# Performance work log

Hardware: AMD Instinct MI355X
Metric: run time of the kernel (lower is better)

Reference implementation:

```python
import jax, jax.numpy as jnp
import numpy as np

B, T, D, NH = 2, 2048, 512, 8
DK = D // NH
P = 2 * T - 1  # relative position length
INIT_SCALE = 0.02


def rel_shift(x):
    # x: [B, H, T, P] -> Transformer-XL pad/reshape shift
    b, h, t, p = x.shape
    x = jnp.pad(x, ((0, 0), (0, 0), (0, 0), (1, 0)))
    x = x.reshape(b, h, p + 1, t)[:, :, 1:]
    return x.reshape(b, h, t, p)


def setup_inputs() -> dict:
    key = jax.random.key(0)
    ks = jax.random.split(key, 7)
    return {
        "x": jax.random.normal(ks[0], (B, T, D), jnp.float32),
        "pos_emb": jax.random.normal(ks[1], (1, P, D), jnp.float32),
        "attn_mask": jnp.zeros((B, T, T), dtype=bool),
        "W_qkv": jax.random.normal(ks[2], (3 * D, D), jnp.float32) * INIT_SCALE,
        "W_pos": jax.random.normal(ks[3], (D, D), jnp.float32) * INIT_SCALE,
        "W_out": jax.random.normal(ks[4], (D, D), jnp.float32) * INIT_SCALE,
        "pos_bias_u": jax.random.normal(ks[5], (NH, DK), jnp.float32) * INIT_SCALE,
        "pos_bias_v": jax.random.normal(ks[6], (NH, DK), jnp.float32) * INIT_SCALE,
    }


def reference(x, pos_emb, attn_mask, W_qkv, W_pos, W_out, pos_bias_u, pos_bias_v):
    b, t, d = x.shape
    nh, dk = pos_bias_u.shape
    scale = 1.0 / np.sqrt(dk).astype(np.float32)
    mask = attn_mask[:, None]  # [B,1,T,T], True = masked

    qkv = x @ W_qkv.T  # [B,T,3D]
    q, k, v = jnp.split(qkv, 3, axis=-1)
    q = q.reshape(b, t, nh, dk)                       # [B,T,H,dk]
    k = k.reshape(b, t, nh, dk).transpose(0, 2, 1, 3)  # [B,H,T,dk]
    v = v.reshape(b, t, nh, dk).transpose(0, 2, 1, 3)  # [B,H,T,dk]

    # pos_emb batch dim is 1 -> squeeze
    pos = (pos_emb @ W_pos.T).reshape(-1, nh, dk).transpose(1, 0, 2)  # [H,P,dk]

    q_u = (q + pos_bias_u).transpose(0, 2, 1, 3)  # [B,H,T,dk]
    q_v = (q + pos_bias_v).transpose(0, 2, 1, 3)  # [B,H,T,dk]

    # relative-position bias: [B,H,T,P] -> shift -> slice to key length
    bd = jnp.einsum("bhtd,hpd->bhtp", q_v, pos)
    bd = rel_shift(bd)[..., :t] * scale
    bd = jnp.where(mask, jnp.float32(-100000.0), bd)

    # SDPA with additive bias (scale = 1/sqrt(dk), matching torch default)
    scores = jnp.einsum("bhtd,bhsd->bhts", q_u, k) * scale + bd
    attn = jax.nn.softmax(scores, axis=-1)
    out = jnp.einsum("bhts,bhsd->bhtd", attn, v)
    out = out.transpose(0, 2, 1, 3)  # [B,T,H,dk]

    # zero fully-masked query rows
    fully_masked = jnp.all(mask, axis=-1)[:, 0]  # [B,T]
    out = jnp.where(fully_masked[:, :, None, None], 0.0, out)

    out = out.reshape(b, t, nh * dk)
    return out @ W_out.T
```

## Files before the change

### kernel.cpp

```cpp
#include <hip/hip_runtime.h>
#include <hip/hip_bf16.h>


typedef __attribute__((ext_vector_type(8))) short short8;
typedef __attribute__((ext_vector_type(16))) float f32x16;
typedef __attribute__((ext_vector_type(4))) float f32x4;
typedef __attribute__((ext_vector_type(2))) unsigned int uint2v;

#define C2F 0.18033688011112043f
#define MOFF 144269.504088896f

static __device__ __forceinline__ unsigned short f2bf(float x) {
    unsigned int u = __builtin_bit_cast(unsigned int, x);
    u += 0x7FFFu + ((u >> 16) & 1u);
    return (unsigned short)(u >> 16);
}
static __device__ __forceinline__ unsigned int cvt2bf(float lo, float hi) {
    __hip_bfloat162 h = __float22bfloat162_rn(make_float2(lo, hi));
    unsigned int r;
    __builtin_memcpy(&r, &h, 4);
    return r;
}
static __device__ __forceinline__ float exp2v(float x) {
    return __builtin_amdgcn_exp2f(x);
}
static __device__ __forceinline__ float bf2f(unsigned short u) {
    return __builtin_bit_cast(float, (unsigned int)u << 16);
}
static __device__ __forceinline__ f32x16 zero16() {
    f32x16 v;
#pragma unroll
    for (int i = 0; i < 16; ++i) v[i] = 0.0f;
    return v;
}
static __device__ __forceinline__ f32x16 mfma_bf(short8 a, short8 b, f32x16 c) {
    return __builtin_amdgcn_mfma_f32_32x32x16_bf16(a, b, c, 0, 0, 0);
}
static __device__ __forceinline__ short8 load8f(const float* base, size_t eoff) {
    const float4* p = (const float4*)(base + eoff);
    float4 a = p[0], b = p[1];
    union { unsigned int u[4]; short8 s; } r;
    r.u[0] = cvt2bf(a.x, a.y);
    r.u[1] = cvt2bf(a.z, a.w);
    r.u[2] = cvt2bf(b.x, b.y);
    r.u[3] = cvt2bf(b.z, b.w);
    return r.s;
}

__global__ __launch_bounds__(256) void front_kernel(
    const float* __restrict__ x, const float* __restrict__ wqkv,
    const float* __restrict__ pe, const float* __restrict__ wpos,
    unsigned short* __restrict__ qu, unsigned short* __restrict__ qv,
    unsigned short* __restrict__ kb, unsigned short* __restrict__ vt,
    unsigned short* __restrict__ posb,
    const float* __restrict__ bu, const float* __restrict__ bv,
    const unsigned char* __restrict__ mk, unsigned long long* __restrict__ mwout)
{
    const int tid = threadIdx.x;
    const int bid = blockIdx.x;

    if (bid >= 512) {
        int base = (bid - 512) * 256 + tid;
#pragma unroll 1
        for (int idx = base; idx < 131072; idx += 32768) {
            const unsigned long long* row =
                (const unsigned long long*)(mk + (size_t)(idx >> 5) * 2048) +
                (size_t)(idx & 31) * 8;
            unsigned long long w = 0;
#pragma unroll
            for (int k = 0; k < 8; ++k) {
                unsigned long long v = row[k];
                v |= v >> 4; v |= v >> 2; v |= v >> 1;
                v &= 0x0101010101010101ull;
                w |= ((v * 0x0102040810204080ull) >> 56) << (k * 8);
            }
            mwout[idx] = w;
        }
        return;
    }

    const int role = bid >= 384 ? 1 : 0;
    const int lb = role ? bid - 384 : bid;
    const int bx = role ? (lb & 3) : (lb % 12);
    const int by = role ? (lb >> 2) : (lb / 12);
    const float* A  = role ? pe : x;
    const float* Bw = role ? wpos : wqkv;
    const int M = role ? 4095 : 4096;

    __shared__ __align__(16) unsigned short As[128 * 32];
    __shared__ __align__(16) unsigned short Bs[128 * 32];

    const int lane = tid & 63;
    const int l31 = lane & 31;
    const int h = (lane >> 5) & 1;
    const int wid = tid >> 6;
    const int wm = wid >> 1, wn = wid & 1;
    const int m0 = by * 128, n0 = bx * 128;

    f32x16 acc[2][2];
#pragma unroll
    for (int mt = 0; mt < 2; ++mt)
#pragma unroll
        for (int nt = 0; nt < 2; ++nt) acc[mt][nt] = zero16();

    const int row_s = tid >> 2;
    const int q_s = tid & 3;

#pragma unroll 1
    for (int k0 = 0; k0 < 512; k0 += 32) {
        __syncthreads();
#pragma unroll
        for (int rep = 0; rep < 2; ++rep) {
            int row = row_s + rep * 64;
            int ar = m0 + row; if (ar > M - 1) ar = M - 1;
            short8 av = load8f(A, (size_t)ar * 512 + k0 + q_s * 8);
            *(short8*)((char*)As + ((row * 64 + q_s * 16) ^ ((row & 3) << 4))) = av;
            int br = n0 + row;
            short8 bv8 = load8f(Bw, (size_t)br * 512 + k0 + q_s * 8);
            *(short8*)((char*)Bs + ((row * 64 + q_s * 16) ^ ((row & 3) << 4))) = bv8;
        }
        __syncthreads();

        short8 af[2][2], bf[2][2];
#pragma unroll
        for (int mt = 0; mt < 2; ++mt)
#pragma unroll
            for (int ks = 0; ks < 2; ++ks) {
                int row = wm * 64 + mt * 32 + l31;
                af[mt][ks] = *(const short8*)((char*)As +
                    ((row * 64 + ks * 32 + h * 16) ^ ((row & 3) << 4)));
            }
#pragma unroll
        for (int nt = 0; nt < 2; ++nt)
#pragma unroll
            for (int ks = 0; ks < 2; ++ks) {
                int row = wn * 64 + nt * 32 + l31;
                bf[nt][ks] = *(const short8*)((char*)Bs +
                    ((row * 64 + ks * 32 + h * 16) ^ ((row & 3) << 4)));
            }
#pragma unroll
        for (int mt = 0; mt < 2; ++mt)
#pragma unroll
            for (int nt = 0; nt < 2; ++nt)
#pragma unroll
                for (int ks = 0; ks < 2; ++ks)
                    acc[mt][nt] = mfma_bf(af[mt][ks], bf[nt][ks], acc[mt][nt]);
    }

#pragma unroll
    for (int mt = 0; mt < 2; ++mt)
#pragma unroll
        for (int nt = 0; nt < 2; ++nt) {
            int Ncol = n0 + wn * 64 + nt * 32 + l31;
#pragma unroll
            for (int r = 0; r < 16; ++r) {
                int Mrow = m0 + wm * 64 + mt * 32 + (r & 3) + ((r >> 2) << 3) + h * 4;
                float v = acc[mt][nt][r];
                if (role == 0) {
                    int b = Mrow >> 11, t = Mrow & 2047;
                    int sec = Ncol >> 9, hd = (Ncol >> 6) & 7, dk = Ncol & 63;
                    if (sec == 0) {
                        size_t idx = ((size_t)((b * 8 + hd) * 2048 + t)) * 64 + dk;
                        qu[idx] = f2bf((v + bu[hd * 64 + dk]) * C2F);
                        qv[idx] = f2bf((v + bv[hd * 64 + dk]) * C2F);
                    } else if (sec == 1) {
                        kb[((size_t)((b * 8 + hd) * 2048 + t)) * 64 + dk] = f2bf(v);
                    } else {
                        vt[((size_t)((b * 8 + hd) * 64 + dk)) * 2048 + t] = f2bf(v);
                    }
                } else {
                    if (Mrow < M) {
                        int hd = Ncol >> 6, dk = Ncol & 63;
                        posb[((size_t)(hd * 4095 + Mrow)) * 64 + dk] = f2bf(v);
                    }
                }
            }
        }
}

__global__ __launch_bounds__(128) void attn_kernel(
    const unsigned short* __restrict__ qup, const unsigned short* __restrict__ qvp,
    const unsigned short* __restrict__ kp,  const unsigned short* __restrict__ vtp,
    const unsigned short* __restrict__ posp,
    const unsigned long long* __restrict__ mwp,
    unsigned short* __restrict__ opart,
    float* __restrict__ mstat, float* __restrict__ lstat)
{
    const int tb = blockIdx.x, bh = blockIdx.y, scb = blockIdx.z;
    const int b = bh >> 3, head = bh & 7;
    const int t0 = tb * 64;
    const int sc = scb << 10;

    const int lane = threadIdx.x & 63;
    const int l31 = lane & 31;
    const int h = (lane >> 5) & 1;
    const int h4 = h * 4;
    const int wid = threadIdx.x >> 6;

    __shared__ __align__(16) unsigned short Kss[64 * 64];
    __shared__ __align__(16) unsigned short Vts[64 * 64];
    __shared__ __align__(16) float Ew[2 * 32 * 132];

    const unsigned short* posg = posp + (size_t)head * 4095 * 64;
    const unsigned short* kg0 = kp + (size_t)bh * 2048 * 64;
    const unsigned short* vtg = vtp + (size_t)bh * 64 * 2048;
    const int t = t0 + wid * 32 + l31;

    const size_t qoff = ((size_t)bh * 2048 + t) * 64;
    short8 qu_f[4], qv_f[4];
#pragma unroll
    for (int ks = 0; ks < 4; ++ks) {
        qu_f[ks] = *(const short8*)(qup + qoff + ks * 16 + h * 8);
        qv_f[ks] = *(const short8*)(qvp + qoff + ks * 16 + h * 8);
    }

    float* ewp = Ew + (wid * 32 + l31) * 132;

    auto load_pos = [&](int c_r0, short8 (&pf)[8]) {
#pragma unroll
        for (int et = 0; et < 2; ++et) {
            int r = c_r0 + et * 32 + l31;
            r = min(r, 4094);
#pragma unroll
            for (int ks = 0; ks < 4; ++ks)
                pf[et * 4 + ks] = *(const short8*)(posg + (size_t)r * 64 + ks * 16 + h * 8);
        }
    };
    auto e_gemm = [&](const short8 (&pf)[8], int slotb) {
#pragma unroll
        for (int et = 0; et < 2; ++et) {
            f32x16 ea = zero16();
#pragma unroll
            for (int ks = 0; ks < 4; ++ks)
                ea = mfma_bf(pf[et * 4 + ks], qv_f[ks], ea);
#pragma unroll
            for (int qd = 0; qd < 4; ++qd) {
                f32x4 w;
                w[0] = ea[qd * 4 + 0]; w[1] = ea[qd * 4 + 1];
                w[2] = ea[qd * 4 + 2]; w[3] = ea[qd * 4 + 3];
                *(f32x4*)(ewp + slotb + et * 32 + qd * 8 + h4) = w;
            }
        }
    };

    const int c0 = sc + 1984 - t0;
    {
        short8 pf0[8];
        load_pos(c0, pf0);      e_gemm(pf0, c0 & 127);
        load_pos(c0 + 64, pf0); e_gemm(pf0, (c0 + 64) & 127);
    }

    float m = -3.0e38f, lsum = 0.0f;
    f32x16 o_acc[2];
    o_acc[0] = zero16(); o_acc[1] = zero16();

    const int st_row = threadIdx.x >> 3;
    const int st_q = threadIdx.x & 7;
    const size_t mw_base = ((size_t)(b * 2048 + t)) * 32 + (sc >> 6);

#pragma unroll 1
    for (int it = 0; it < 16; ++it) {
        const int s0a = sc + it * 64;
        __syncthreads();
#pragma unroll
        for (int rep = 0; rep < 4; ++rep) {
            int row = st_row + rep * 16;
            int off = (row * 128 + st_q * 16) ^ ((row & 7) << 4);
            *(short8*)((char*)Kss + off) =
                *(const short8*)(kg0 + ((size_t)(s0a + row)) * 64 + st_q * 8);
            *(short8*)((char*)Vts + off) =
                *(const short8*)(vtg + (size_t)row * 2048 + s0a + st_q * 8);
        }
        short8 pf[8];
        if (it < 15) load_pos(c0 + 128 + 64 * it, pf);
        unsigned long long mw = mwp[mw_base + it];
        __syncthreads();

        f32x16 sacc[2];
        sacc[0] = zero16(); sacc[1] = zero16();
#pragma unroll
        for (int st2 = 0; st2 < 2; ++st2)
#pragma unroll
            for (int ks = 0; ks < 4; ++ks) {
                int row = st2 * 32 + l31;
                short8 a = *(const short8*)((char*)Kss +
                    ((row * 128 + ks * 32 + h * 16) ^ ((row & 7) << 4)));
                sacc[st2] = mfma_bf(a, qu_f[ks], sacc[st2]);
            }

        const int sb = s0a - t + 2047;
        float sv[32];
#pragma unroll
        for (int st2 = 0; st2 < 2; ++st2)
#pragma unroll
            for (int r = 0; r < 16; ++r) {
                int slot = (sb + st2 * 32 + (r & 3) + ((r >> 2) << 3) + h4) & 127;
                sv[st2 * 16 + r] = sacc[st2][r] + ewp[slot];
            }
        if (__any(mw != 0ull)) {
#pragma unroll
            for (int st2 = 0; st2 < 2; ++st2)
#pragma unroll
                for (int r = 0; r < 16; ++r) {
                    int s_loc = st2 * 32 + (r & 3) + ((r >> 2) << 3) + h4;
                    if ((mw >> s_loc) & 1ull)
                        sv[st2 * 16 + r] = sacc[st2][r] - MOFF;
                }
        }

        float mx = sv[0];
#pragma unroll
        for (int i = 1; i < 32; ++i) mx = fmaxf(mx, sv[i]);
        mx = fmaxf(mx, __shfl_xor(mx, 32));
        float mnew = fmaxf(m, mx);
        float alpha = exp2v(m - mnew);
        m = mnew;
        float psum = 0.0f;
#pragma unroll
        for (int i = 0; i < 32; ++i) { sv[i] = exp2v(sv[i] - mnew); psum += sv[i]; }
        psum += __shfl_xor(psum, 32);
        lsum = lsum * alpha + psum;
        o_acc[0] = o_acc[0] * alpha;
        o_acc[1] = o_acc[1] * alpha;

        short8 pfrag[4];
#pragma unroll
        for (int st2 = 0; st2 < 2; ++st2) {
            unsigned int X[8];
#pragma unroll
            for (int qd = 0; qd < 4; ++qd) {
                X[qd * 2 + 0] = cvt2bf(sv[st2 * 16 + qd * 4 + 0], sv[st2 * 16 + qd * 4 + 1]);
                X[qd * 2 + 1] = cvt2bf(sv[st2 * 16 + qd * 4 + 2], sv[st2 * 16 + qd * 4 + 3]);
            }
#pragma unroll
            for (int f = 0; f < 2; ++f) {
                unsigned int a0 = X[4 * f + 0], a1 = X[4 * f + 1];
                unsigned int b0 = X[4 * f + 2], b1 = X[4 * f + 3];
                unsigned int sa0 = (unsigned int)__shfl_xor((int)a0, 32);
                unsigned int sa1 = (unsigned int)__shfl_xor((int)a1, 32);
                unsigned int sb0 = (unsigned int)__shfl_xor((int)b0, 32);
                unsigned int sb1 = (unsigned int)__shfl_xor((int)b1, 32);
                union { unsigned int u[4]; short8 s8; } uu;
                uu.u[0] = h ? sb0 : a0;
                uu.u[1] = h ? sb1 : a1;
                uu.u[2] = h ? b0 : sa0;
                uu.u[3] = h ? b1 : sa1;
                pfrag[st2 * 2 + f] = uu.s8;
            }
        }

#pragma unroll
        for (int dkt = 0; dkt < 2; ++dkt)
#pragma unroll
            for (int f = 0; f < 4; ++f) {
                int row = dkt * 32 + l31;
                short8 a = *(const short8*)((char*)Vts +
                    ((row * 128 + f * 32 + h * 16) ^ ((row & 7) << 4)));
                o_acc[dkt] = mfma_bf(a, pfrag[f], o_acc[dkt]);
            }

        if (it < 15) e_gemm(pf, (c0 + 128 + 64 * it) & 127);
    }

    float inv = 1.0f / lsum;
    if (m <= -9.0e4f) inv = 0.0f;
    size_t obase = (((size_t)scb * 16 + bh) * 2048 + t) * 64;
#pragma unroll
    for (int dkt = 0; dkt < 2; ++dkt)
#pragma unroll
        for (int qd = 0; qd < 4; ++qd) {
            int dk0 = dkt * 32 + qd * 8 + h4;
            uint2v u;
            u.x = cvt2bf(o_acc[dkt][qd * 4 + 0] * inv, o_acc[dkt][qd * 4 + 1] * inv);
            u.y = cvt2bf(o_acc[dkt][qd * 4 + 2] * inv, o_acc[dkt][qd * 4 + 3] * inv);
            *(uint2v*)(opart + obase + dk0) = u;
        }
    if (h == 0) {
        size_t sidx = ((size_t)scb * 16 + bh) * 2048 + t;
        mstat[sidx] = m;
        lstat[sidx] = lsum;
    }
}

__global__ __launch_bounds__(256) void back_kernel(
    const unsigned short* __restrict__ opart, const float* __restrict__ wout,
    const float* __restrict__ mstat, const float* __restrict__ lstat,
    float* __restrict__ o_f)
{
    __shared__ __align__(16) unsigned short As[128 * 32];
    __shared__ __align__(16) unsigned short Bs[128 * 32];

    const int tid = threadIdx.x;
    const int lane = tid & 63;
    const int l31 = lane & 31;
    const int h = (lane >> 5) & 1;
    const int wid = tid >> 6;
    const int wm = wid >> 1, wn = wid & 1;
    const int m0 = blockIdx.y * 128, n0 = blockIdx.x * 128;

    f32x16 acc[2][2];
#pragma unroll
    for (int mt = 0; mt < 2; ++mt)
#pragma unroll
        for (int nt = 0; nt < 2; ++nt) acc[mt][nt] = zero16();

    const int row_s = tid >> 2;
    const int q_s = tid & 3;

#pragma unroll 1
    for (int k0 = 0; k0 < 512; k0 += 32) {
        __syncthreads();
#pragma unroll
        for (int rep = 0; rep < 2; ++rep) {
            int row = row_s + rep * 64;
            int ar = m0 + row;
            int t_ = ar & 2047, b_ = ar >> 11;
            int c = k0 + q_s * 8;
            int head = c >> 6, dk0 = c & 63;
            int row2 = (b_ * 8 + head) * 2048 + t_;
            float m0s = mstat[row2], m1s = mstat[32768 + row2];
            float l0s = lstat[row2], l1s = lstat[32768 + row2];
            float Mx = fmaxf(m0s, m1s);
            float w0 = exp2v(m0s - Mx) * l0s, w1 = exp2v(m1s - Mx) * l1s;
            float den = w0 + w1;
            float inv = (den > 0.0f && Mx > -9.0e4f) ? 1.0f / den : 0.0f;
            w0 *= inv; w1 *= inv;
            short8 p0 = *(const short8*)(opart + (size_t)row2 * 64 + dk0);
            short8 p1 = *(const short8*)(opart + ((size_t)32768 + row2) * 64 + dk0);
            union { unsigned int u[4]; short8 s; } r;
#pragma unroll
            for (int j = 0; j < 4; ++j) {
                float lo = w0 * bf2f((unsigned short)p0[2 * j]) +
                           w1 * bf2f((unsigned short)p1[2 * j]);
                float hi = w0 * bf2f((unsigned short)p0[2 * j + 1]) +
                           w1 * bf2f((unsigned short)p1[2 * j + 1]);
                r.u[j] = cvt2bf(lo, hi);
            }
            *(short8*)((char*)As + ((row * 64 + q_s * 16) ^ ((row & 3) << 4))) = r.s;
            int br = n0 + row;
            short8 bv8 = load8f(wout, (size_t)br * 512 + k0 + q_s * 8);
            *(short8*)((char*)Bs + ((row * 64 + q_s * 16) ^ ((row & 3) << 4))) = bv8;
        }
        __syncthreads();

        short8 af[2][2], bf[2][2];
#pragma unroll
        for (int mt = 0; mt < 2; ++mt)
#pragma unroll
            for (int ks = 0; ks < 2; ++ks) {
                int row = wm * 64 + mt * 32 + l31;
                af[mt][ks] = *(const short8*)((char*)As +
                    ((row * 64 + ks * 32 + h * 16) ^ ((row & 3) << 4)));
            }
#pragma unroll
        for (int nt = 0; nt < 2; ++nt)
#pragma unroll
            for (int ks = 0; ks < 2; ++ks) {
                int row = wn * 64 + nt * 32 + l31;
                bf[nt][ks] = *(const short8*)((char*)Bs +
                    ((row * 64 + ks * 32 + h * 16) ^ ((row & 3) << 4)));
            }
#pragma unroll
        for (int mt = 0; mt < 2; ++mt)
#pragma unroll
            for (int nt = 0; nt < 2; ++nt)
#pragma unroll
                for (int ks = 0; ks < 2; ++ks)
                    acc[mt][nt] = mfma_bf(af[mt][ks], bf[nt][ks], acc[mt][nt]);
    }

#pragma unroll
    for (int mt = 0; mt < 2; ++mt)
#pragma unroll
        for (int nt = 0; nt < 2; ++nt) {
            int Ncol = n0 + wn * 64 + nt * 32 + l31;
#pragma unroll
            for (int r = 0; r < 16; ++r) {
                int Mrow = m0 + wm * 64 + mt * 32 + (r & 3) + ((r >> 2) << 3) + h * 4;
                o_f[(size_t)Mrow * 512 + Ncol] = acc[mt][nt][r];
            }
        }
}

extern "C" void kernel_launch(void* const* d_in, const int* in_sizes, int n_in,
                              void* d_out, int out_size, void* d_ws, size_t ws_size,
                              hipStream_t stream) {
    const float* x    = (const float*)d_in[0];
    const float* pe   = (const float*)d_in[1];
    const unsigned char* mask = (const unsigned char*)d_in[2];
    const float* wqkv = (const float*)d_in[3];
    const float* wpos = (const float*)d_in[4];
    const float* wout = (const float*)d_in[5];
    const float* bu   = (const float*)d_in[6];
    const float* bv   = (const float*)d_in[7];
    float* out = (float*)d_out;

    char* ws = (char*)d_ws;
    unsigned short* qu    = (unsigned short*)(ws + 0);
    unsigned short* qv    = (unsigned short*)(ws + 4194304);
    unsigned short* kb    = (unsigned short*)(ws + 8388608);
    unsigned short* vt    = (unsigned short*)(ws + 12582912);
    unsigned short* posb  = (unsigned short*)(ws + 16777216);
    unsigned long long* maskw = (unsigned long long*)(ws + 20971520);
    unsigned short* opart = (unsigned short*)(ws + 22020096);
    float* mstat          = (float*)(ws + 30408704);
    float* lstat          = (float*)(ws + 30670848);

    front_kernel<<<640, 256, 0, stream>>>(
        x, wqkv, pe, wpos, qu, qv, kb, vt, posb, bu, bv, mask, maskw);
    attn_kernel<<<dim3(32, 16, 2), 128, 0, stream>>>(
        qu, qv, kb, vt, posb, maskw, opart, mstat, lstat);
    back_kernel<<<dim3(4, 32), 256, 0, stream>>>(
        opart, wout, mstat, lstat, out);
}
```

Before: 147.8 us.

## Prefetch next K/V tile into registers and tree-reduce softmax max/sum

K and V tile loads from global memory now go into registers one iteration ahead, so the shared-memory write at the top of each iteration no longer waits on global latency. Position-embedding fragments are also prefetched an iteration earlier. The row max and sum reductions are rewritten as pairwise trees to shorten the dependency chain. The prefetch raises register pressure, which may lower occupancy.

New measurement: 153.4 us. +3.8%, slower.

```diff
diff --git a/kernel.cpp b/kernel.cpp
--- a/kernel.cpp
+++ b/kernel.cpp
@@ -243,38 +243,53 @@
         }
     };
 
+    const int st_row = threadIdx.x >> 3;
+    const int st_q = threadIdx.x & 7;
+
+    auto stage_issue = [&](int it, short8 (&kr)[4], short8 (&vr)[4]) {
+        const int s0a = sc + it * 64;
+#pragma unroll
+        for (int rep = 0; rep < 4; ++rep) {
+            int row = st_row + rep * 16;
+            kr[rep] = *(const short8*)(kg0 + ((size_t)(s0a + row)) * 64 + st_q * 8);
+            vr[rep] = *(const short8*)(vtg + (size_t)row * 2048 + s0a + st_q * 8);
+        }
+    };
+    auto stage_write = [&](const short8 (&kr)[4], const short8 (&vr)[4]) {
+#pragma unroll
+        for (int rep = 0; rep < 4; ++rep) {
+            int row = st_row + rep * 16;
+            int off = (row * 128 + st_q * 16) ^ ((row & 7) << 4);
+            *(short8*)((char*)Kss + off) = kr[rep];
+            *(short8*)((char*)Vts + off) = vr[rep];
+        }
+    };
+
     const int c0 = sc + 1984 - t0;
+    short8 kr[4], vr[4], pf[8];
+    stage_issue(0, kr, vr);
     {
         short8 pf0[8];
         load_pos(c0, pf0);      e_gemm(pf0, c0 & 127);
         load_pos(c0 + 64, pf0); e_gemm(pf0, (c0 + 64) & 127);
     }
+    load_pos(c0 + 128, pf);
 
     float m = -3.0e38f, lsum = 0.0f;
     f32x16 o_acc[2];
     o_acc[0] = zero16(); o_acc[1] = zero16();
 
-    const int st_row = threadIdx.x >> 3;
-    const int st_q = threadIdx.x & 7;
     const size_t mw_base = ((size_t)(b * 2048 + t)) * 32 + (sc >> 6);
 
 #pragma unroll 1
     for (int it = 0; it < 16; ++it) {
-        const int s0a = sc + it * 64;
         __syncthreads();
-#pragma unroll
-        for (int rep = 0; rep < 4; ++rep) {
-            int row = st_row + rep * 16;
-            int off = (row * 128 + st_q * 16) ^ ((row & 7) << 4);
-            *(short8*)((char*)Kss + off) =
-                *(const short8*)(kg0 + ((size_t)(s0a + row)) * 64 + st_q * 8);
-            *(short8*)((char*)Vts + off) =
-                *(const short8*)(vtg + (size_t)row * 2048 + s0a + st_q * 8);
-        }
-        short8 pf[8];
-        if (it < 15) load_pos(c0 + 128 + 64 * it, pf);
+        stage_write(kr, vr);
         unsigned long long mw = mwp[mw_base + it];
         __syncthreads();
+        if (it < 15) {
+            stage_issue(it + 1, kr, vr);
+        }
 
         f32x16 sacc[2];
         sacc[0] = zero16(); sacc[1] = zero16();
@@ -288,6 +303,7 @@
                 sacc[st2] = mfma_bf(a, qu_f[ks], sacc[st2]);
             }
 
+        const int s0a = sc + it * 64;
         const int sb = s0a - t + 2047;
         float sv[32];
 #pragma unroll
@@ -308,17 +324,31 @@
                 }
         }
 
-        float mx = sv[0];
-#pragma unroll
-        for (int i = 1; i < 32; ++i) mx = fmaxf(mx, sv[i]);
-        mx = fmaxf(mx, __shfl_xor(mx, 32));
+        float tm[16];
+#pragma unroll
+        for (int i = 0; i < 16; ++i) tm[i] = fmaxf(sv[i], sv[i + 16]);
+#pragma unroll
+        for (int s2 = 8; s2 > 0; s2 >>= 1)
+#pragma unroll
+            for (int i = 0; i < 8; ++i)
+                if (i < s2) tm[i] = fmaxf(tm[i], tm[i + s2]);
+        float mx = fmaxf(tm[0], __shfl_xor(tm[0], 32));
         float mnew = fmaxf(m, mx);
         float alpha = exp2v(m - mnew);
         m = mnew;
-        float psum = 0.0f;
-#pragma unroll
-        for (int i = 0; i < 32; ++i) { sv[i] = exp2v(sv[i] - mnew); psum += sv[i]; }
-        psum += __shfl_xor(psum, 32);
+        float ts[16];
+#pragma unroll
+        for (int i = 0; i < 16; ++i) {
+            sv[i] = exp2v(sv[i] - mnew);
+            sv[i + 16] = exp2v(sv[i + 16] - mnew);
+            ts[i] = sv[i] + sv[i + 16];
+        }
+#pragma unroll
+        for (int s2 = 8; s2 > 0; s2 >>= 1)
+#pragma unroll
+            for (int i = 0; i < 8; ++i)
+                if (i < s2) ts[i] += ts[i + s2];
+        float psum = ts[0] + __shfl_xor(ts[0], 32);
         lsum = lsum * alpha + psum;
         o_acc[0] = o_acc[0] * alpha;
         o_acc[1] = o_acc[1] * alpha;
@@ -359,7 +389,10 @@
                 o_acc[dkt] = mfma_bf(a, pfrag[f], o_acc[dkt]);
             }
 
-        if (it < 15) e_gemm(pf, (c0 + 128 + 64 * it) & 127);
+        if (it < 15) {
+            e_gemm(pf, (c0 + 128 + 64 * it) & 127);
+            if (it < 14) load_pos(c0 + 192 + 64 * it, pf);
+        }
     }
 
     float inv = 1.0f / lsum;
```
